# Kernel tuning notes

Measured on AMD Instinct MI355X. Metric: run time of the kernel, lower is better.

## Reference

```python
import jax, jax.numpy as jnp
import numpy as np

EPS = 1e-5

def layer_norm(x, g, b):
    mu = jnp.mean(x, axis=-1, keepdims=True)
    var = jnp.mean(jnp.square(x - mu), axis=-1, keepdims=True)
    return (x - mu) * jax.lax.rsqrt(var + EPS) * g + b

def gather_recent(seq_tokens, seq_mask, count):
    # vectorized right-aligned gather of last `count` valid tokens per row
    B, S, D = seq_tokens.shape
    csum = jnp.cumsum(seq_mask.astype(jnp.int32), axis=1)          # [B,S]
    total = csum[:, -1:]                                           # [B,1]
    rank = total - csum                                            # 0 = last valid (at valid positions)
    sel = seq_mask & (rank < count)
    dest = jnp.where(sel, count - 1 - rank, count)                 # dump invalid into slot `count`
    b_idx = jnp.arange(B)[:, None]
    buf = jnp.zeros((B, count + 1, D), seq_tokens.dtype)
    recent = buf.at[b_idx, dest].set(seq_tokens * sel[..., None].astype(seq_tokens.dtype))[:, :count]
    recent_mask = jnp.arange(count)[None, :] >= (count - total)    # [B,count]
    return recent, recent_mask

def setup_inputs() -> dict:
    key = jax.random.key(0)
    B, S, D, H, P = 16, 2048, 1024, 16, 8
    ks = jax.random.split(key, 8)
    hidden_states = jax.random.normal(ks[0], (B, S, D), jnp.float32)
    lengths = jax.random.randint(ks[1], (B,), 1, S + 1)
    valid_mask = jnp.arange(S)[None, :] < lengths[:, None]
    s = 0.02
    return {
        "hidden_states": hidden_states,
        "valid_mask": valid_mask,
        "queries": jax.random.normal(ks[2], (P, D), jnp.float32) * s,
        "in_proj_w": jax.random.normal(ks[3], (3 * D, D), jnp.float32) * s,
        "in_proj_b": jnp.zeros((3 * D,), jnp.float32),
        "out_w": jax.random.normal(ks[4], (D, D), jnp.float32) * s,
        "out_b": jnp.zeros((D,), jnp.float32),
        "ln_pma_g": jnp.ones((D,), jnp.float32),
        "ln_pma_b": jnp.zeros((D,), jnp.float32),
        "ln_v_g": jnp.ones((D,), jnp.float32),
        "ln_v_b": jnp.zeros((D,), jnp.float32),
        "W_v": jax.random.normal(ks[5], (D, D), jnp.float32) * s,
        "b_v": jnp.zeros((D,), jnp.float32),
        "ln_g_g": jnp.ones((D,), jnp.float32),
        "ln_g_b": jnp.zeros((D,), jnp.float32),
        "W_g": jax.random.normal(ks[6], (D, D), jnp.float32) * s,
        "b_g": jnp.zeros((D,), jnp.float32),
        "cls_count": 1, "pma_count": 8, "recent_count": 64, "num_heads": 16,
    }

def reference(hidden_states, valid_mask, queries, in_proj_w, in_proj_b, out_w, out_b,
              ln_pma_g, ln_pma_b, ln_v_g, ln_v_b, W_v, b_v, ln_g_g, ln_g_b, W_g, b_g,
              cls_count, pma_count, recent_count, num_heads):
    B, S, D = hidden_states.shape
    H = num_heads
    hd = D // H
    # ---- PMA (torch nn.MultiheadAttention, batch_first, eval/no-dropout) ----
    Wq, Wk, Wv_ = in_proj_w[:D], in_proj_w[D:2 * D], in_proj_w[2 * D:]
    bq, bk, bv_ = in_proj_b[:D], in_proj_b[D:2 * D], in_proj_b[2 * D:]
    q = (queries @ Wq.T + bq)                       # [P, D]
    k = hidden_states @ Wk.T + bk                   # [B, S, D]
    v = hidden_states @ Wv_.T + bv_                 # [B, S, D]
    qh = q.reshape(pma_count, H, hd)                # [P, H, hd]
    kh = k.reshape(B, S, H, hd)
    vh = v.reshape(B, S, H, hd)
    scores = jnp.einsum('phd,bshd->bhps', qh, kh) / jnp.sqrt(jnp.asarray(hd, hidden_states.dtype))
    scores = jnp.where(valid_mask[:, None, None, :], scores, jnp.asarray(-1e9, scores.dtype))
    attn = jax.nn.softmax(scores, axis=-1)          # [B, H, P, S]
    ctx = jnp.einsum('bhps,bshd->bphd', attn, vh).reshape(B, pma_count, D)
    pooled = ctx @ out_w.T + out_b
    pma_tokens = layer_norm(queries[None, :, :] + pooled, ln_pma_g, ln_pma_b)  # [B, P, D]
    pma_mask = jnp.ones((B, pma_count), bool)
    # ---- split cls / sequence, gather recent ----
    cls_tokens = hidden_states[:, :cls_count]
    cls_mask = valid_mask[:, :cls_count]
    recent_tokens, recent_mask = gather_recent(hidden_states[:, cls_count:],
                                               valid_mask[:, cls_count:], recent_count)
    summary = jnp.concatenate([cls_tokens, pma_tokens, recent_tokens], axis=1)
    summary_mask = jnp.concatenate([cls_mask, pma_mask, recent_mask], axis=1)
    # ---- SiLU self-gating ----
    val = jax.nn.silu(layer_norm(summary, ln_v_g, ln_v_b) @ W_v.T + b_v)
    gate = jax.nn.sigmoid(layer_norm(summary, ln_g_g, ln_g_b) @ W_g.T + b_g)
    gated = gate * val * summary_mask[..., None].astype(summary.dtype)
    return gated, summary_mask
```

## Files before the change

kernel.cpp:

```cpp
#include <hip/hip_runtime.h>
#include <hip/hip_bf16.h>
#include <math.h>


#define Bn 16
#define Sn 2048
#define Dn 1024
#define Hn 16
#define Pn 8
#define Tn 73
#define RECn 64

typedef __attribute__((ext_vector_type(8))) short short8;
typedef __attribute__((ext_vector_type(4))) float f32x4;

__device__ __forceinline__ short f2bf(float x) {
    union { __hip_bfloat16 h; short s; } u;
    u.h = __float2bfloat16(x);
    return u.s;
}

__global__ void detect_mask_kernel(const unsigned char* __restrict__ raw,
                                   int* __restrict__ flag) {
    __shared__ int any;
    if (threadIdx.x == 0) any = 0;
    __syncthreads();
    const uint4* r4 = (const uint4*)raw;
    int local = 0;
    for (int i = threadIdx.x; i < (Bn * Sn) / 16; i += blockDim.x) {
        uint4 w = r4[i];
        if ((w.x & 0xFFFFFF00u) | (w.y & 0xFFFFFF00u) |
            (w.z & 0xFFFFFF00u) | (w.w & 0xFFFFFF00u)) local = 1;
    }
    if (local) any = 1;
    __syncthreads();
    if (threadIdx.x == 0) *flag = any;
}

__global__ void canon_mask_kernel(const void* __restrict__ raw,
                                  const int* __restrict__ flag,
                                  unsigned char* __restrict__ canon) {
    int i = blockIdx.x * blockDim.x + threadIdx.x;
    if (i >= Bn * Sn) return;
    unsigned char v;
    if (*flag)
        v = ((const unsigned char*)raw)[i] ? 1 : 0;
    else
        v = ((const int*)raw)[i] ? 1 : 0;
    canon[i] = v;
}

__global__ void prep_kernel(const unsigned char* __restrict__ valid,
                            int* __restrict__ totals, int* __restrict__ rsrc,
                            float* __restrict__ maskf) {
    int b = blockIdx.x, t = threadIdx.x;
    const int SP = Sn - 1;
    __shared__ int lc[256];
    if (t < RECn) rsrc[b * RECn + t] = -1;

    int base = t * 8;
    unsigned char m[8];
    int cnt = 0;
#pragma unroll
    for (int i = 0; i < 8; i++) {
        int idx = base + i;
        m[i] = (idx < SP) ? valid[(size_t)b * Sn + 1 + idx] : (unsigned char)0;
        cnt += m[i] ? 1 : 0;
    }
    lc[t] = cnt;
    __syncthreads();
    for (int off = 1; off < 256; off <<= 1) {
        int add = (t >= off) ? lc[t - off] : 0;
        __syncthreads();
        lc[t] += add;
        __syncthreads();
    }
    int total = lc[255];
    int run = lc[t] - cnt;
#pragma unroll
    for (int i = 0; i < 8; i++) {
        if (m[i]) {
            run++;
            int rank = total - run;
            if (rank < RECn) rsrc[b * RECn + (RECn - 1 - rank)] = base + i + 1;
        }
    }
    if (t == 0) totals[b] = total;
    if (t < Tn) {
        float mv;
        if (t == 0) mv = valid[(size_t)b * Sn] ? 1.0f : 0.0f;
        else if (t < 1 + Pn) mv = 1.0f;
        else mv = ((t - 9) >= RECn - total) ? 1.0f : 0.0f;
        maskf[b * Tn + t] = mv;
    }
}

__global__ void q_kernel(const float* __restrict__ queries,
                         const float* __restrict__ in_w,
                         const float* __restrict__ in_b,
                         float* __restrict__ q) {
    int wid = (blockIdx.x * blockDim.x + threadIdx.x) >> 6;
    int lane = threadIdx.x & 63;
    if (wid >= Pn * Dn) return;
    int p = wid >> 10, j = wid & 1023;
    float acc = 0.0f;
    for (int c = lane; c < Dn; c += 64)
        acc += queries[p * Dn + c] * in_w[(size_t)j * Dn + c];
#pragma unroll
    for (int off = 32; off > 0; off >>= 1) acc += __shfl_down(acc, off);
    if (lane == 0) q[wid] = acc + in_b[j];
}

__global__ void A_kernel(const float* __restrict__ q,
                         const float* __restrict__ in_w,
                         const float* __restrict__ in_b,
                         short* __restrict__ Amat_bf, float* __restrict__ c0) {
    int h = blockIdx.x, cblk = blockIdx.y;
    int c = cblk * 256 + threadIdx.x;
    __shared__ float qs[8][64];
    for (int i = threadIdx.x; i < 512; i += 256) {
        int p = i >> 6, d = i & 63;
        qs[p][d] = q[p * Dn + h * 64 + d];
    }
    __syncthreads();
    float acc[8] = {};
#pragma unroll 8
    for (int d = 0; d < 64; d++) {
        float w = in_w[(size_t)(Dn + h * 64 + d) * Dn + c];
#pragma unroll
        for (int p = 0; p < 8; p++) acc[p] = fmaf(qs[p][d], w, acc[p]);
    }
#pragma unroll
    for (int p = 0; p < 8; p++)
        Amat_bf[(size_t)(h * 8 + p) * Dn + c] = f2bf(acc[p] * 0.125f);
    if (cblk == 0 && threadIdx.x < 8) {
        int p = threadIdx.x;
        float a = 0.0f;
        for (int d = 0; d < 64; d++) a += qs[p][d] * in_b[Dn + h * 64 + d];
        c0[h * 8 + p] = a * 0.125f;
    }
}

__global__ void wcvt_kernel(const float* __restrict__ w, short* __restrict__ wbf, int n) {
    int i = (blockIdx.x * blockDim.x + threadIdx.x) * 8;
    if (i >= n) return;
    f32x4 x0 = *(const f32x4*)(w + i);
    f32x4 x1 = *(const f32x4*)(w + i + 4);
    short8 o;
#pragma unroll
    for (int j = 0; j < 4; j++) { o[j] = f2bf(x0[j]); o[j + 4] = f2bf(x1[j]); }
    *(short8*)(wbf + i) = o;
}

__global__ __launch_bounds__(256) void scores_mfma(const float* __restrict__ hidden,
                                                   const short* __restrict__ Amat_bf,
                                                   const float* __restrict__ c0,
                                                   const unsigned char* __restrict__ valid,
                                                   float* __restrict__ scores) {
    int tid = threadIdx.x, wave = tid >> 6, lane = tid & 63;
    int l15 = lane & 15, koff = (lane >> 4) * 8;
    int mrow0 = blockIdx.x * 32 + (wave >> 1) * 16;
    int hpbase = (wave & 1) * 64;
    int b = mrow0 >> 11, s_base = mrow0 & 2047;

    __shared__ short Ab[2][128][40];
    int shp = tid >> 1, skp = (tid & 1) * 16;
    const short* aglob = Amat_bf + (size_t)shp * Dn + skp;
    const float* hptr = hidden + (size_t)(mrow0 + l15) * Dn + koff;

    f32x4 acc[4] = {};
    {
        short8 s0 = *(const short8*)(aglob);
        short8 s1 = *(const short8*)(aglob + 8);
        *(short8*)(&Ab[0][shp][skp]) = s0;
        *(short8*)(&Ab[0][shp][skp + 8]) = s1;
    }
    f32x4 ha = *(const f32x4*)(hptr);
    f32x4 hb = *(const f32x4*)(hptr + 4);
    f32x4 ha1 = *(const f32x4*)(hptr + 32);
    f32x4 hb1 = *(const f32x4*)(hptr + 36);

    for (int ic = 0; ic < 32; ic++) {
        int cur = ic & 1;
        short8 nA0 = {}, nA1 = {};
        f32x4 nh0 = {}, nh1 = {};
        if (ic + 1 < 32) {
            nA0 = *(const short8*)(aglob + (ic + 1) * 32);
            nA1 = *(const short8*)(aglob + (ic + 1) * 32 + 8);
        }
        if (ic + 2 < 32) {
            nh0 = *(const f32x4*)(hptr + (ic + 2) * 32);
            nh1 = *(const f32x4*)(hptr + (ic + 2) * 32 + 4);
        }
        __syncthreads();
        short8 av;
#pragma unroll
        for (int i = 0; i < 4; i++) { av[i] = f2bf(ha[i]); av[i + 4] = f2bf(hb[i]); }
#pragma unroll
        for (int nt = 0; nt < 4; nt++) {
            short8 bv = *(const short8*)(&Ab[cur][hpbase + nt * 16 + l15][koff]);
            acc[nt] = __builtin_amdgcn_mfma_f32_16x16x32_bf16(av, bv, acc[nt], 0, 0, 0);
        }
        if (ic + 1 < 32) {
            *(short8*)(&Ab[cur ^ 1][shp][skp]) = nA0;
            *(short8*)(&Ab[cur ^ 1][shp][skp + 8]) = nA1;
        }
        ha = ha1; hb = hb1; ha1 = nh0; hb1 = nh1;
    }
    int srow = s_base + (lane >> 4) * 4;
    const unsigned char* vptr = valid + (size_t)b * Sn + srow;
    bool ok0 = vptr[0] != 0, ok1 = vptr[1] != 0, ok2 = vptr[2] != 0, ok3 = vptr[3] != 0;
#pragma unroll
    for (int nt = 0; nt < 4; nt++) {
        int hp = hpbase + nt * 16 + l15;
        float cc = c0[hp];
        f32x4 st;
        st[0] = ok0 ? acc[nt][0] + cc : -1.0e9f;
        st[1] = ok1 ? acc[nt][1] + cc : -1.0e9f;
        st[2] = ok2 ? acc[nt][2] + cc : -1.0e9f;
        st[3] = ok3 ? acc[nt][3] + cc : -1.0e9f;
        *(f32x4*)(scores + (size_t)(b * 128 + hp) * Sn + srow) = st;
    }
}

__global__ __launch_bounds__(256) void softmax_kernel(const float* __restrict__ scores,
                                                      short* __restrict__ attn_bf) {
    const float* row = scores + (size_t)blockIdx.x * Sn;
    short* orow = attn_bf + (size_t)blockIdx.x * Sn;
    int t = threadIdx.x;
    __shared__ float red[256];
    f32x4 v0 = *(const f32x4*)(row + t * 8);
    f32x4 v1 = *(const f32x4*)(row + t * 8 + 4);
    float mx = -1.0e30f;
#pragma unroll
    for (int i = 0; i < 4; i++) { mx = fmaxf(mx, v0[i]); mx = fmaxf(mx, v1[i]); }
    red[t] = mx;
    __syncthreads();
    for (int off = 128; off > 0; off >>= 1) {
        if (t < off) red[t] = fmaxf(red[t], red[t + off]);
        __syncthreads();
    }
    mx = red[0];
    __syncthreads();
    float e[8];
    float sum = 0.0f;
#pragma unroll
    for (int i = 0; i < 4; i++) {
        e[i] = expf(v0[i] - mx); sum += e[i];
        e[i + 4] = expf(v1[i] - mx); sum += e[i + 4];
    }
    red[t] = sum;
    __syncthreads();
    for (int off = 128; off > 0; off >>= 1) {
        if (t < off) red[t] += red[t + off];
        __syncthreads();
    }
    float inv = 1.0f / red[0];
    short8 o;
#pragma unroll
    for (int i = 0; i < 8; i++) o[i] = f2bf(e[i] * inv);
    *(short8*)(orow + t * 8) = o;
}

__global__ __launch_bounds__(512) void U_mfma(const short* __restrict__ attn_bf,
                                              const float* __restrict__ hidden,
                                              float* __restrict__ Up0,
                                              float* __restrict__ Up1,
                                              float* __restrict__ Up2,
                                              float* __restrict__ Up3) {
    int b = blockIdx.y, n0 = blockIdx.x * 128, z = blockIdx.z;
    int zbase = z * 512;
    float* Up = (z == 0) ? Up0 : (z == 1) ? Up1 : (z == 2) ? Up2 : Up3;

    int tid = threadIdx.x, wave = tid >> 6, lane = tid & 63;
    int l15 = lane & 15;
    __shared__ short ldsB[2][128][40];
    int kr = tid & 31, nc = (tid >> 5) * 8;
    int koff = (lane >> 4) * 8;
    f32x4 acc[8] = {};
    const short* aBase = attn_bf + ((size_t)b * 128 + wave * 16 + l15) * Sn + zbase + koff;
    const float* hBase = hidden + ((size_t)b * Sn + zbase + kr) * Dn + n0 + nc;

    const int nk = 16;
    f32x4 h0 = *(const f32x4*)(hBase);
    f32x4 h1 = *(const f32x4*)(hBase + 4);
#pragma unroll
    for (int i = 0; i < 4; i++) {
        ldsB[0][nc + i][kr] = f2bf(h0[i]);
        ldsB[0][nc + 4 + i][kr] = f2bf(h1[i]);
    }
    short8 av = *(const short8*)(aBase);

    for (int ic = 0; ic < nk; ic++) {
        int cur = ic & 1;
        bool more = (ic + 1 < nk);
        f32x4 hn0, hn1;
        short8 avn;
        if (more) {
            hn0 = *(const f32x4*)(hBase + (size_t)(ic + 1) * 32 * Dn);
            hn1 = *(const f32x4*)(hBase + (size_t)(ic + 1) * 32 * Dn + 4);
            avn = *(const short8*)(aBase + (ic + 1) * 32);
        }
        __syncthreads();
#pragma unroll
        for (int nf = 0; nf < 8; nf++) {
            short8 bv = *(const short8*)(&ldsB[cur][nf * 16 + l15][koff]);
            acc[nf] = __builtin_amdgcn_mfma_f32_16x16x32_bf16(av, bv, acc[nf], 0, 0, 0);
        }
        if (more) {
#pragma unroll
            for (int i = 0; i < 4; i++) {
                ldsB[cur ^ 1][nc + i][kr] = f2bf(hn0[i]);
                ldsB[cur ^ 1][nc + 4 + i][kr] = f2bf(hn1[i]);
            }
            av = avn;
        }
    }
    int hp = wave * 16 + (lane >> 4) * 4;
#pragma unroll
    for (int nf = 0; nf < 8; nf++) {
        int c = n0 + nf * 16 + l15;
        float* up = Up + (size_t)(b * 128 + hp) * Dn + c;
#pragma unroll
        for (int r = 0; r < 4; r++) up[(size_t)r * Dn] = acc[nf][r];
    }
}

__global__ __launch_bounds__(64) void ctx_mfma(const float* __restrict__ Up0,
                                               const float* __restrict__ Up1,
                                               const float* __restrict__ Up2,
                                               const float* __restrict__ Up3,
                                               const float* __restrict__ in_w,
                                               const float* __restrict__ in_b,
                                               float* __restrict__ ctx) {
    int bh = blockIdx.x, b = bh >> 4, h = bh & 15;
    int lane = threadIdx.x & 63, l15 = lane & 15, koff = (lane >> 4) * 8;
    int p = l15 & 7;
    size_t uoff = ((size_t)b * 128 + h * 8 + p) * Dn + koff;
    const float* wv = in_w + (size_t)(2 * Dn + h * 64 + l15) * Dn + koff;
    f32x4 acc[4] = {};
    for (int k0 = 0; k0 < Dn; k0 += 32) {
        f32x4 a0 = *(const f32x4*)(Up0 + uoff + k0);
        f32x4 a1 = *(const f32x4*)(Up0 + uoff + k0 + 4);
        f32x4 b0 = *(const f32x4*)(Up1 + uoff + k0);
        f32x4 b1 = *(const f32x4*)(Up1 + uoff + k0 + 4);
        f32x4 d0 = *(const f32x4*)(Up2 + uoff + k0);
        f32x4 d1 = *(const f32x4*)(Up2 + uoff + k0 + 4);
        f32x4 e0 = *(const f32x4*)(Up3 + uoff + k0);
        f32x4 e1 = *(const f32x4*)(Up3 + uoff + k0 + 4);
        short8 av;
#pragma unroll
        for (int i = 0; i < 4; i++) {
            av[i] = f2bf((a0[i] + b0[i]) + (d0[i] + e0[i]));
            av[i + 4] = f2bf((a1[i] + b1[i]) + (d1[i] + e1[i]));
        }
#pragma unroll
        for (int nt = 0; nt < 4; nt++) {
            f32x4 w0 = *(const f32x4*)(wv + (size_t)nt * 16 * Dn + k0);
            f32x4 w1 = *(const f32x4*)(wv + (size_t)nt * 16 * Dn + k0 + 4);
            short8 bv;
#pragma unroll
            for (int i = 0; i < 4; i++) { bv[i] = f2bf(w0[i]); bv[i + 4] = f2bf(w1[i]); }
            acc[nt] = __builtin_amdgcn_mfma_f32_16x16x32_bf16(av, bv, acc[nt], 0, 0, 0);
        }
    }
    if (lane < 32) {
        int prow = (lane >> 4) * 4;
#pragma unroll
        for (int nt = 0; nt < 4; nt++) {
            int d = h * 64 + nt * 16 + l15;
            float bias = in_b[2 * Dn + d];
#pragma unroll
            for (int r = 0; r < 4; r++)
                ctx[(size_t)(b * 8 + prow + r) * Dn + d] = acc[nt][r] + bias;
        }
    }
}

__global__ __launch_bounds__(256) void pooled_mfma(const float* __restrict__ A,
                                                   const float* __restrict__ B,
                                                   const float* __restrict__ bias,
                                                   float* __restrict__ C, int M) {
    int wave = threadIdx.x >> 6, lane = threadIdx.x & 63;
    int l15 = lane & 15, koff = (lane >> 4) * 8;
    int m0 = blockIdx.x * 64 + (wave >> 1) * 32;
    int n0 = blockIdx.y * 64 + (wave & 1) * 32;
    f32x4 acc[2][2] = {};
    int ra0 = min(m0 + l15, M - 1);
    int ra1 = min(m0 + 16 + l15, M - 1);
    const float* a0p = A + (size_t)ra0 * Dn + koff;
    const float* a1p = A + (size_t)ra1 * Dn + koff;
    const float* b0p = B + (size_t)(n0 + l15) * Dn + koff;
    const float* b1p = B + (size_t)(n0 + 16 + l15) * Dn + koff;
    for (int k0 = 0; k0 < Dn; k0 += 32) {
        short8 av0, av1, bv0, bv1;
        f32x4 x, y;
        x = *(const f32x4*)(a0p + k0); y = *(const f32x4*)(a0p + k0 + 4);
#pragma unroll
        for (int i = 0; i < 4; i++) { av0[i] = f2bf(x[i]); av0[i + 4] = f2bf(y[i]); }
        x = *(const f32x4*)(a1p + k0); y = *(const f32x4*)(a1p + k0 + 4);
#pragma unroll
        for (int i = 0; i < 4; i++) { av1[i] = f2bf(x[i]); av1[i + 4] = f2bf(y[i]); }
        x = *(const f32x4*)(b0p + k0); y = *(const f32x4*)(b0p + k0 + 4);
#pragma unroll
        for (int i = 0; i < 4; i++) { bv0[i] = f2bf(x[i]); bv0[i + 4] = f2bf(y[i]); }
        x = *(const f32x4*)(b1p + k0); y = *(const f32x4*)(b1p + k0 + 4);
#pragma unroll
        for (int i = 0; i < 4; i++) { bv1[i] = f2bf(x[i]); bv1[i + 4] = f2bf(y[i]); }
        acc[0][0] = __builtin_amdgcn_mfma_f32_16x16x32_bf16(av0, bv0, acc[0][0], 0, 0, 0);
        acc[0][1] = __builtin_amdgcn_mfma_f32_16x16x32_bf16(av0, bv1, acc[0][1], 0, 0, 0);
        acc[1][0] = __builtin_amdgcn_mfma_f32_16x16x32_bf16(av1, bv0, acc[1][0], 0, 0, 0);
        acc[1][1] = __builtin_amdgcn_mfma_f32_16x16x32_bf16(av1, bv1, acc[1][1], 0, 0, 0);
    }
#pragma unroll
    for (int mf = 0; mf < 2; mf++) {
        int row0 = m0 + mf * 16 + (lane >> 4) * 4;
#pragma unroll
        for (int nf = 0; nf < 2; nf++) {
            int col = n0 + nf * 16 + l15;
            float bval = bias[col];
#pragma unroll
            for (int r = 0; r < 4; r++) {
                int row = row0 + r;
                if (row < M) C[(size_t)row * Dn + col] = acc[mf][nf][r] + bval;
            }
        }
    }
}

__global__ __launch_bounds__(256) void wgemm_mfma(const short* __restrict__ Abf,
                                                  const short* __restrict__ Bbf,
                                                  const float* __restrict__ bias,
                                                  float* __restrict__ C, int M) {
    int wave = threadIdx.x >> 6, lane = threadIdx.x & 63;
    int m0 = blockIdx.x * 64 + (wave >> 1) * 32;
    int n0 = blockIdx.y * 64 + (wave & 1) * 32;
    int koff = (lane >> 4) * 8;
    f32x4 acc[2][2] = {};
    int ra0 = min(m0 + (lane & 15), M - 1);
    int ra1 = min(m0 + 16 + (lane & 15), M - 1);
    const short* a0p = Abf + (size_t)ra0 * Dn + koff;
    const short* a1p = Abf + (size_t)ra1 * Dn + koff;
    const short* b0p = Bbf + (size_t)(n0 + (lane & 15)) * Dn + koff;
    const short* b1p = Bbf + (size_t)(n0 + 16 + (lane & 15)) * Dn + koff;
    for (int k0 = 0; k0 < Dn; k0 += 32) {
        short8 av0 = *(const short8*)(a0p + k0);
        short8 av1 = *(const short8*)(a1p + k0);
        short8 bv0 = *(const short8*)(b0p + k0);
        short8 bv1 = *(const short8*)(b1p + k0);
        acc[0][0] = __builtin_amdgcn_mfma_f32_16x16x32_bf16(av0, bv0, acc[0][0], 0, 0, 0);
        acc[0][1] = __builtin_amdgcn_mfma_f32_16x16x32_bf16(av0, bv1, acc[0][1], 0, 0, 0);
        acc[1][0] = __builtin_amdgcn_mfma_f32_16x16x32_bf16(av1, bv0, acc[1][0], 0, 0, 0);
        acc[1][1] = __builtin_amdgcn_mfma_f32_16x16x32_bf16(av1, bv1, acc[1][1], 0, 0, 0);
    }
#pragma unroll
    for (int mf = 0; mf < 2; mf++) {
        int row0 = m0 + mf * 16 + (lane >> 4) * 4;
#pragma unroll
        for (int nf = 0; nf < 2; nf++) {
            int col = n0 + nf * 16 + (lane & 15);
            float bval = bias[col];
#pragma unroll
            for (int r = 0; r < 4; r++) {
                int row = row0 + r;
                if (row < M) C[(size_t)row * Dn + col] = acc[mf][nf][r] + bval;
            }
        }
    }
}

__device__ __forceinline__ float block_sum(float v, float* red) {
    int tid = threadIdx.x;
    red[tid] = v;
    __syncthreads();
    for (int off = 128; off > 0; off >>= 1) {
        if (tid < off) red[tid] += red[tid + off];
        __syncthreads();
    }
    float r = red[0];
    __syncthreads();
    return r;
}

__global__ void summary_ln_kernel(const float* __restrict__ hidden,
                                  const float* __restrict__ queries,
                                  const float* __restrict__ pooled,
                                  const int* __restrict__ rsrc,
                                  const float* __restrict__ gpma, const float* __restrict__ bpma,
                                  const float* __restrict__ gv, const float* __restrict__ bv,
                                  const float* __restrict__ gg, const float* __restrict__ bg,
                                  short* __restrict__ lnv, short* __restrict__ lng) {
    __shared__ float red[256];
    int b = blockIdx.x, t = blockIdx.y, tid = threadIdx.x;
    float x[4];
    if (t == 0) {
#pragma unroll
        for (int i = 0; i < 4; i++)
            x[i] = hidden[(size_t)b * Sn * Dn + tid + i * 256];
    } else if (t < 1 + Pn) {
        int p = t - 1;
#pragma unroll
        for (int i = 0; i < 4; i++) {
            int c = tid + i * 256;
            x[i] = queries[p * Dn + c] + pooled[((size_t)b * Pn + p) * Dn + c];
        }
    } else {
        int src = rsrc[b * RECn + (t - 9)];
        if (src >= 0) {
#pragma unroll
            for (int i = 0; i < 4; i++)
                x[i] = hidden[((size_t)b * Sn + src) * Dn + tid + i * 256];
        } else {
#pragma unroll
            for (int i = 0; i < 4; i++) x[i] = 0.0f;
        }
    }
    if (t >= 1 && t < 1 + Pn) {
        float mu = block_sum(x[0] + x[1] + x[2] + x[3], red) * (1.0f / Dn);
        float d2 = 0.0f;
#pragma unroll
        for (int i = 0; i < 4; i++) { float d = x[i] - mu; d2 += d * d; }
        float inv = rsqrtf(block_sum(d2, red) * (1.0f / Dn) + 1e-5f);
#pragma unroll
        for (int i = 0; i < 4; i++) {
            int c = tid + i * 256;
            x[i] = (x[i] - mu) * inv * gpma[c] + bpma[c];
        }
    }
    float mu = block_sum(x[0] + x[1] + x[2] + x[3], red) * (1.0f / Dn);
    float d2 = 0.0f;
#pragma unroll
    for (int i = 0; i < 4; i++) { float d = x[i] - mu; d2 += d * d; }
    float inv = rsqrtf(block_sum(d2, red) * (1.0f / Dn) + 1e-5f);
    size_t row = (size_t)(b * Tn + t) * Dn;
#pragma unroll
    for (int i = 0; i < 4; i++) {
        int c = tid + i * 256;
        float xh = (x[i] - mu) * inv;
        lnv[row + c] = f2bf(xh * gv[c] + bv[c]);
        lng[row + c] = f2bf(xh * gg[c] + bg[c]);
    }
}

__global__ void gated_kernel(const float* __restrict__ c1, const float* __restrict__ c2,
                             const float* __restrict__ maskf, float* __restrict__ out) {
    int gi = blockIdx.x * blockDim.x + threadIdx.x;
    int row = gi >> 10;
    float m = maskf[row];
    float a = c1[gi], g = c2[gi];
    float sv = a / (1.0f + expf(-a));
    float sg = 1.0f / (1.0f + expf(-g));
    out[gi] = sg * sv * m;
}

extern "C" void kernel_launch(void* const* d_in, const int* in_sizes, int n_in,
                              void* d_out, int out_size, void* d_ws, size_t ws_size,
                              hipStream_t stream) {
    const float* hidden = (const float*)d_in[0];
    const void* valid_raw = d_in[1];
    const float* queries = (const float*)d_in[2];
    const float* in_w = (const float*)d_in[3];
    const float* in_b = (const float*)d_in[4];
    const float* out_w = (const float*)d_in[5];
    const float* out_b = (const float*)d_in[6];
    const float* ln_pma_g = (const float*)d_in[7];
    const float* ln_pma_b = (const float*)d_in[8];
    const float* ln_v_g = (const float*)d_in[9];
    const float* ln_v_b = (const float*)d_in[10];
    const float* W_v = (const float*)d_in[11];
    const float* b_v = (const float*)d_in[12];
    const float* ln_g_g = (const float*)d_in[13];
    const float* ln_g_b = (const float*)d_in[14];
    const float* W_g = (const float*)d_in[15];
    const float* b_g = (const float*)d_in[16];

    float* ws = (float*)d_ws;
    float* out = (float*)d_out;

    float* SC      = ws;
    short* attn_bf = (short*)(ws + 4194304);
    float* Up0     = ws + 6291456;
    float* Up1     = ws;
    float* Up2     = ws + 2097152;
    float* Up3     = ws + 8388608;
    float* qbuf    = ws + 10485760;
    short* Amat_bf = (short*)(ws + 10493952);
    float* c0      = ws + 10559488;
    float* ctx     = ws + 10559744;
    float* pooled  = ws + 10690816;
    short* Wv_bf   = (short*)(ws + 10821888);
    short* Wg_bf   = (short*)(ws + 11346176);
    int*   ivals   = (int*)(ws + 11870464);
    int* totals = ivals;
    int* rsrc = ivals + 16;
    int* flag = ivals + 16 + 1024;
    unsigned char* canon = (unsigned char*)(ivals + 16 + 1024 + 16);
    short* lnv_bf = (short*)ws;
    short* lng_bf = (short*)(ws + 622592);
    float* c1 = ws + 1245184;
    float* c2 = ws + 2441216;
    float* maskf = out + (size_t)Bn * Tn * Dn;

    const int M2 = Bn * Tn;

    detect_mask_kernel<<<1, 256, 0, stream>>>((const unsigned char*)valid_raw, flag);
    canon_mask_kernel<<<(Bn * Sn) / 256, 256, 0, stream>>>(valid_raw, flag, canon);
    prep_kernel<<<Bn, 256, 0, stream>>>(canon, totals, rsrc, maskf);
    q_kernel<<<(Pn * Dn) / 4, 256, 0, stream>>>(queries, in_w, in_b, qbuf);
    A_kernel<<<dim3(Hn, 4), 256, 0, stream>>>(qbuf, in_w, in_b, Amat_bf, c0);
    wcvt_kernel<<<512, 256, 0, stream>>>(W_v, Wv_bf, Dn * Dn);
    wcvt_kernel<<<512, 256, 0, stream>>>(W_g, Wg_bf, Dn * Dn);
    scores_mfma<<<(Bn * Sn) / 32, 256, 0, stream>>>(hidden, Amat_bf, c0, canon, SC);
    softmax_kernel<<<Bn * 128, 256, 0, stream>>>(SC, attn_bf);
    U_mfma<<<dim3(8, Bn, 4), 512, 0, stream>>>(attn_bf, hidden, Up0, Up1, Up2, Up3);
    ctx_mfma<<<Bn * Hn, 64, 0, stream>>>(Up0, Up1, Up2, Up3, in_w, in_b, ctx);
    pooled_mfma<<<dim3(2, 16), 256, 0, stream>>>(ctx, out_w, out_b, pooled, Bn * Pn);
    summary_ln_kernel<<<dim3(Bn, Tn), 256, 0, stream>>>(hidden, queries, pooled, rsrc,
                                                        ln_pma_g, ln_pma_b, ln_v_g, ln_v_b,
                                                        ln_g_g, ln_g_b, lnv_bf, lng_bf);
    wgemm_mfma<<<dim3((M2 + 63) / 64, 16), 256, 0, stream>>>(lnv_bf, Wv_bf, b_v, c1, M2);
    wgemm_mfma<<<dim3((M2 + 63) / 64, 16), 256, 0, stream>>>(lng_bf, Wg_bf, b_g, c2, M2);
    gated_kernel<<<(Bn * Tn * Dn) / 256, 256, 0, stream>>>(c1, c2, maskf, out);
}
```

Before: 260.2 us.

## Stage full K-half tiles in swizzled LDS for scores and U GEMMs

scores_mfma now runs as a split-K GEMM over two halves with 512 threads. It loads the whole 128x512 bf16 A-matrix slice into XOR-swizzled shared memory once, writes two partial score buffers, and leaves the bias add and masking to the softmax kernel. U_mfma similarly converts and stages its entire 512x128 hidden tile into swizzled LDS up front, replacing the per-step double-buffered loop with its barriers. This drops per-iteration syncs and bank conflicts and lets each block reuse more data. In exchange it uses 128 KB of LDS per block, which limits occupancy, and it adds extra partial-score traffic to global memory.

Result: faster. 249.2 us (-4.2%).

```diff
diff --git a/kernel.cpp b/kernel.cpp
--- a/kernel.cpp
+++ b/kernel.cpp
@@ -18,6 +18,10 @@
     union { __hip_bfloat16 h; short s; } u;
     u.h = __float2bfloat16(x);
     return u.s;
+}
+
+__device__ __forceinline__ int swz(int row, int ks) {
+    return row * 512 + (ks ^ ((row & 7) << 3));
 }
 
 __global__ void detect_mask_kernel(const unsigned char* __restrict__ raw,
@@ -152,88 +156,85 @@
     *(short8*)(wbf + i) = o;
 }
 
-__global__ __launch_bounds__(256) void scores_mfma(const float* __restrict__ hidden,
+__global__ __launch_bounds__(512) void scores_mfma(const float* __restrict__ hidden,
                                                    const short* __restrict__ Amat_bf,
-                                                   const float* __restrict__ c0,
-                                                   const unsigned char* __restrict__ valid,
-                                                   float* __restrict__ scores) {
+                                                   float* __restrict__ SCp0,
+                                                   float* __restrict__ SCp1) {
+    __shared__ short Bsh[128 * 512];
     int tid = threadIdx.x, wave = tid >> 6, lane = tid & 63;
-    int l15 = lane & 15, koff = (lane >> 4) * 8;
-    int mrow0 = blockIdx.x * 32 + (wave >> 1) * 16;
-    int hpbase = (wave & 1) * 64;
-    int b = mrow0 >> 11, s_base = mrow0 & 2047;
-
-    __shared__ short Ab[2][128][40];
-    int shp = tid >> 1, skp = (tid & 1) * 16;
-    const short* aglob = Amat_bf + (size_t)shp * Dn + skp;
-    const float* hptr = hidden + (size_t)(mrow0 + l15) * Dn + koff;
-
-    f32x4 acc[4] = {};
+    int l15 = lane & 15, q = lane >> 4;
+    int kz = blockIdx.y, khalf = kz << 9;
+    float* SCp = kz ? SCp1 : SCp0;
+    int m0 = blockIdx.x * 128 + wave * 16;
+    int b = m0 >> 11, s_base = m0 & 2047;
+
     {
-        short8 s0 = *(const short8*)(aglob);
-        short8 s1 = *(const short8*)(aglob + 8);
-        *(short8*)(&Ab[0][shp][skp]) = s0;
-        *(short8*)(&Ab[0][shp][skp + 8]) = s1;
-    }
-    f32x4 ha = *(const f32x4*)(hptr);
-    f32x4 hb = *(const f32x4*)(hptr + 4);
-    f32x4 ha1 = *(const f32x4*)(hptr + 32);
-    f32x4 hb1 = *(const f32x4*)(hptr + 36);
-
-    for (int ic = 0; ic < 32; ic++) {
-        int cur = ic & 1;
-        short8 nA0 = {}, nA1 = {};
-        f32x4 nh0 = {}, nh1 = {};
-        if (ic + 1 < 32) {
-            nA0 = *(const short8*)(aglob + (ic + 1) * 32);
-            nA1 = *(const short8*)(aglob + (ic + 1) * 32 + 8);
-        }
-        if (ic + 2 < 32) {
-            nh0 = *(const f32x4*)(hptr + (ic + 2) * 32);
-            nh1 = *(const f32x4*)(hptr + (ic + 2) * 32 + 4);
-        }
-        __syncthreads();
+        int r = tid >> 2, k0 = (tid & 3) * 128;
+        const short* src = Amat_bf + (size_t)r * Dn + khalf + k0;
+#pragma unroll
+        for (int j = 0; j < 16; j++) {
+            short8 v = *(const short8*)(src + j * 8);
+            *(short8*)(&Bsh[swz(r, k0 + j * 8)]) = v;
+        }
+    }
+    __syncthreads();
+
+    const float* aptr = hidden + (size_t)(m0 + l15) * Dn + khalf + q * 8;
+    f32x4 acc[8] = {};
+    f32x4 pa[2][2];
+    pa[0][0] = *(const f32x4*)(aptr);       pa[0][1] = *(const f32x4*)(aptr + 4);
+    pa[1][0] = *(const f32x4*)(aptr + 32);  pa[1][1] = *(const f32x4*)(aptr + 36);
+#pragma unroll 4
+    for (int ic = 0; ic < 16; ic++) {
+        f32x4 c0r = pa[ic & 1][0], c1r = pa[ic & 1][1];
+        if (ic + 2 < 16) {
+            pa[ic & 1][0] = *(const f32x4*)(aptr + (ic + 2) * 32);
+            pa[ic & 1][1] = *(const f32x4*)(aptr + (ic + 2) * 32 + 4);
+        }
         short8 av;
 #pragma unroll
-        for (int i = 0; i < 4; i++) { av[i] = f2bf(ha[i]); av[i + 4] = f2bf(hb[i]); }
-#pragma unroll
-        for (int nt = 0; nt < 4; nt++) {
-            short8 bv = *(const short8*)(&Ab[cur][hpbase + nt * 16 + l15][koff]);
+        for (int i = 0; i < 4; i++) { av[i] = f2bf(c0r[i]); av[i + 4] = f2bf(c1r[i]); }
+#pragma unroll
+        for (int nt = 0; nt < 8; nt++) {
+            short8 bv = *(const short8*)(&Bsh[swz(nt * 16 + l15, ic * 32 + q * 8)]);
             acc[nt] = __builtin_amdgcn_mfma_f32_16x16x32_bf16(av, bv, acc[nt], 0, 0, 0);
         }
-        if (ic + 1 < 32) {
-            *(short8*)(&Ab[cur ^ 1][shp][skp]) = nA0;
-            *(short8*)(&Ab[cur ^ 1][shp][skp + 8]) = nA1;
-        }
-        ha = ha1; hb = hb1; ha1 = nh0; hb1 = nh1;
-    }
-    int srow = s_base + (lane >> 4) * 4;
-    const unsigned char* vptr = valid + (size_t)b * Sn + srow;
-    bool ok0 = vptr[0] != 0, ok1 = vptr[1] != 0, ok2 = vptr[2] != 0, ok3 = vptr[3] != 0;
-#pragma unroll
-    for (int nt = 0; nt < 4; nt++) {
-        int hp = hpbase + nt * 16 + l15;
-        float cc = c0[hp];
-        f32x4 st;
-        st[0] = ok0 ? acc[nt][0] + cc : -1.0e9f;
-        st[1] = ok1 ? acc[nt][1] + cc : -1.0e9f;
-        st[2] = ok2 ? acc[nt][2] + cc : -1.0e9f;
-        st[3] = ok3 ? acc[nt][3] + cc : -1.0e9f;
-        *(f32x4*)(scores + (size_t)(b * 128 + hp) * Sn + srow) = st;
-    }
-}
-
-__global__ __launch_bounds__(256) void softmax_kernel(const float* __restrict__ scores,
+    }
+    int srow = s_base + q * 4;
+#pragma unroll
+    for (int nt = 0; nt < 8; nt++) {
+        int hp = nt * 16 + l15;
+        *(f32x4*)(SCp + (size_t)(b * 128 + hp) * Sn + srow) = acc[nt];
+    }
+}
+
+__global__ __launch_bounds__(256) void softmax_kernel(const float* __restrict__ p0,
+                                                      const float* __restrict__ p1,
+                                                      const float* __restrict__ c0,
+                                                      const unsigned char* __restrict__ valid,
                                                       short* __restrict__ attn_bf) {
-    const float* row = scores + (size_t)blockIdx.x * Sn;
-    short* orow = attn_bf + (size_t)blockIdx.x * Sn;
+    int rowid = blockIdx.x;
+    int b = rowid >> 7, hp = rowid & 127;
+    const float* r0 = p0 + (size_t)rowid * Sn;
+    const float* r1 = p1 + (size_t)rowid * Sn;
+    const unsigned char* vp = valid + (size_t)b * Sn;
+    short* orow = attn_bf + (size_t)rowid * Sn;
     int t = threadIdx.x;
+    float cc = c0[hp];
     __shared__ float red[256];
-    f32x4 v0 = *(const f32x4*)(row + t * 8);
-    f32x4 v1 = *(const f32x4*)(row + t * 8 + 4);
+    f32x4 a0 = *(const f32x4*)(r0 + t * 8);
+    f32x4 a1 = *(const f32x4*)(r0 + t * 8 + 4);
+    f32x4 b0 = *(const f32x4*)(r1 + t * 8);
+    f32x4 b1 = *(const f32x4*)(r1 + t * 8 + 4);
+    float v[8];
+#pragma unroll
+    for (int i = 0; i < 4; i++) {
+        v[i] = (vp[t * 8 + i] != 0) ? (a0[i] + b0[i] + cc) : -1.0e9f;
+        v[i + 4] = (vp[t * 8 + 4 + i] != 0) ? (a1[i] + b1[i] + cc) : -1.0e9f;
+    }
     float mx = -1.0e30f;
 #pragma unroll
-    for (int i = 0; i < 4; i++) { mx = fmaxf(mx, v0[i]); mx = fmaxf(mx, v1[i]); }
+    for (int i = 0; i < 8; i++) mx = fmaxf(mx, v[i]);
     red[t] = mx;
     __syncthreads();
     for (int off = 128; off > 0; off >>= 1) {
@@ -242,13 +243,9 @@
     }
     mx = red[0];
     __syncthreads();
-    float e[8];
     float sum = 0.0f;
 #pragma unroll
-    for (int i = 0; i < 4; i++) {
-        e[i] = expf(v0[i] - mx); sum += e[i];
-        e[i + 4] = expf(v1[i] - mx); sum += e[i + 4];
-    }
+    for (int i = 0; i < 8; i++) { v[i] = expf(v[i] - mx); sum += v[i]; }
     red[t] = sum;
     __syncthreads();
     for (int off = 128; off > 0; off >>= 1) {
@@ -258,7 +255,7 @@
     float inv = 1.0f / red[0];
     short8 o;
 #pragma unroll
-    for (int i = 0; i < 8; i++) o[i] = f2bf(e[i] * inv);
+    for (int i = 0; i < 8; i++) o[i] = f2bf(v[i] * inv);
     *(short8*)(orow + t * 8) = o;
 }
 
@@ -268,55 +265,47 @@
                                               float* __restrict__ Up1,
                                               float* __restrict__ Up2,
                                               float* __restrict__ Up3) {
-    int b = blockIdx.y, n0 = blockIdx.x * 128, z = blockIdx.z;
+    __shared__ short Hs[128 * 512];
+    int n0 = blockIdx.x * 128, b = blockIdx.y, z = blockIdx.z;
     int zbase = z * 512;
     float* Up = (z == 0) ? Up0 : (z == 1) ? Up1 : (z == 2) ? Up2 : Up3;
-
     int tid = threadIdx.x, wave = tid >> 6, lane = tid & 63;
-    int l15 = lane & 15;
-    __shared__ short ldsB[2][128][40];
-    int kr = tid & 31, nc = (tid >> 5) * 8;
-    int koff = (lane >> 4) * 8;
+    int l15 = lane & 15, q = lane >> 4;
+
+    {
+        const float* src = hidden + ((size_t)b * Sn + zbase + tid) * Dn + n0;
+#pragma unroll 4
+        for (int c = 0; c < 128; c += 8) {
+            f32x4 x = *(const f32x4*)(src + c);
+            f32x4 y = *(const f32x4*)(src + c + 4);
+#pragma unroll
+            for (int i = 0; i < 4; i++) {
+                Hs[swz(c + i, 0) + ((tid ^ (((c + i) & 7) << 3)) - (0 ^ (((c + i) & 7) << 3)))] = f2bf(x[i]);
+            }
+#pragma unroll
+            for (int i = 0; i < 4; i++) {
+                Hs[(c + 4 + i) * 512 + (tid ^ (((c + 4 + i) & 7) << 3))] = f2bf(y[i]);
+            }
+        }
+    }
+    __syncthreads();
+
+    const short* ap = attn_bf + ((size_t)b * 128 + wave * 16 + l15) * Sn + zbase + q * 8;
     f32x4 acc[8] = {};
-    const short* aBase = attn_bf + ((size_t)b * 128 + wave * 16 + l15) * Sn + zbase + koff;
-    const float* hBase = hidden + ((size_t)b * Sn + zbase + kr) * Dn + n0 + nc;
-
-    const int nk = 16;
-    f32x4 h0 = *(const f32x4*)(hBase);
-    f32x4 h1 = *(const f32x4*)(hBase + 4);
-#pragma unroll
-    for (int i = 0; i < 4; i++) {
-        ldsB[0][nc + i][kr] = f2bf(h0[i]);
-        ldsB[0][nc + 4 + i][kr] = f2bf(h1[i]);
-    }
-    short8 av = *(const short8*)(aBase);
-
-    for (int ic = 0; ic < nk; ic++) {
-        int cur = ic & 1;
-        bool more = (ic + 1 < nk);
-        f32x4 hn0, hn1;
-        short8 avn;
-        if (more) {
-            hn0 = *(const f32x4*)(hBase + (size_t)(ic + 1) * 32 * Dn);
-            hn1 = *(const f32x4*)(hBase + (size_t)(ic + 1) * 32 * Dn + 4);
-            avn = *(const short8*)(aBase + (ic + 1) * 32);
-        }
-        __syncthreads();
+    short8 pa[2];
+    pa[0] = *(const short8*)(ap);
+    pa[1] = *(const short8*)(ap + 32);
+#pragma unroll 4
+    for (int ic = 0; ic < 16; ic++) {
+        short8 av = pa[ic & 1];
+        if (ic + 2 < 16) pa[ic & 1] = *(const short8*)(ap + (ic + 2) * 32);
 #pragma unroll
         for (int nf = 0; nf < 8; nf++) {
-            short8 bv = *(const short8*)(&ldsB[cur][nf * 16 + l15][koff]);
+            short8 bv = *(const short8*)(&Hs[swz(nf * 16 + l15, ic * 32 + q * 8)]);
             acc[nf] = __builtin_amdgcn_mfma_f32_16x16x32_bf16(av, bv, acc[nf], 0, 0, 0);
         }
-        if (more) {
-#pragma unroll
-            for (int i = 0; i < 4; i++) {
-                ldsB[cur ^ 1][nc + i][kr] = f2bf(hn0[i]);
-                ldsB[cur ^ 1][nc + 4 + i][kr] = f2bf(hn1[i]);
-            }
-            av = avn;
-        }
-    }
-    int hp = wave * 16 + (lane >> 4) * 4;
+    }
+    int hp = wave * 16 + q * 4;
 #pragma unroll
     for (int nf = 0; nf < 8; nf++) {
         int c = n0 + nf * 16 + l15;
@@ -577,12 +566,13 @@
     float* ws = (float*)d_ws;
     float* out = (float*)d_out;
 
-    float* SC      = ws;
-    short* attn_bf = (short*)(ws + 4194304);
-    float* Up0     = ws + 6291456;
-    float* Up1     = ws;
-    float* Up2     = ws + 2097152;
-    float* Up3     = ws + 8388608;
+    float* SCp0    = ws;
+    float* SCp1    = ws + 4194304;
+    short* attn_bf = (short*)(ws + 8388608);
+    float* Up0     = ws;
+    float* Up1     = ws + 2097152;
+    float* Up2     = ws + 4194304;
+    float* Up3     = ws + 6291456;
     float* qbuf    = ws + 10485760;
     short* Amat_bf = (short*)(ws + 10493952);
     float* c0      = ws + 10559488;
@@ -610,8 +600,8 @@
     A_kernel<<<dim3(Hn, 4), 256, 0, stream>>>(qbuf, in_w, in_b, Amat_bf, c0);
     wcvt_kernel<<<512, 256, 0, stream>>>(W_v, Wv_bf, Dn * Dn);
     wcvt_kernel<<<512, 256, 0, stream>>>(W_g, Wg_bf, Dn * Dn);
-    scores_mfma<<<(Bn * Sn) / 32, 256, 0, stream>>>(hidden, Amat_bf, c0, canon, SC);
-    softmax_kernel<<<Bn * 128, 256, 0, stream>>>(SC, attn_bf);
+    scores_mfma<<<dim3(256, 2), 512, 0, stream>>>(hidden, Amat_bf, SCp0, SCp1);
+    softmax_kernel<<<Bn * 128, 256, 0, stream>>>(SCp0, SCp1, c0, canon, attn_bf);
     U_mfma<<<dim3(8, Bn, 4), 512, 0, stream>>>(attn_bf, hidden, Up0, Up1, Up2, Up3);
     ctx_mfma<<<Bn * Hn, 64, 0, stream>>>(Up0, Up1, Up2, Up3, in_w, in_b, ctx);
     pooled_mfma<<<dim3(2, 16), 256, 0, stream>>>(ctx, out_w, out_b, pooled, Bn * Pn);
```

## Retile scores and U GEMMs with large swizzled LDS tiles and deeper prefetch

Applied to the files above, without the earlier changes.

The scores GEMM now uses 512-thread blocks covering 128 rows. Each block stages a 256-wide K slab of the bf16 query-key matrix in XOR-swizzled LDS, double-buffered, and prefetches the hidden-state A operand four K-steps ahead. The U GEMM now converts a whole 512x64 hidden tile to bf16 in swizzled LDS once, then streams the attention rows from registers, with no per-step barriers. The aim is fewer syncs, fewer LDS bank conflicts and more reuse per block, at the cost of much larger LDS use per block (128KB and 64KB), which limits occupancy. The Up buffer aliasing in the workspace is also rearranged.

Result: faster. 254.1 us (-2.3%).

```diff
diff --git a/kernel.cpp b/kernel.cpp
--- a/kernel.cpp
+++ b/kernel.cpp
@@ -18,6 +18,10 @@
     union { __hip_bfloat16 h; short s; } u;
     u.h = __float2bfloat16(x);
     return u.s;
+}
+
+__device__ __forceinline__ int swzP(int row, int ks, int pitch) {
+    return row * pitch + (ks ^ ((row & 7) << 3));
 }
 
 __global__ void detect_mask_kernel(const unsigned char* __restrict__ raw,
@@ -152,67 +156,78 @@
     *(short8*)(wbf + i) = o;
 }
 
-__global__ __launch_bounds__(256) void scores_mfma(const float* __restrict__ hidden,
+__global__ __launch_bounds__(512) void scores_mfma(const float* __restrict__ hidden,
                                                    const short* __restrict__ Amat_bf,
                                                    const float* __restrict__ c0,
                                                    const unsigned char* __restrict__ valid,
                                                    float* __restrict__ scores) {
+    __shared__ short Bsh[2][64 * 512];
     int tid = threadIdx.x, wave = tid >> 6, lane = tid & 63;
-    int l15 = lane & 15, koff = (lane >> 4) * 8;
-    int mrow0 = blockIdx.x * 32 + (wave >> 1) * 16;
-    int hpbase = (wave & 1) * 64;
-    int b = mrow0 >> 11, s_base = mrow0 & 2047;
-
-    __shared__ short Ab[2][128][40];
-    int shp = tid >> 1, skp = (tid & 1) * 16;
-    const short* aglob = Amat_bf + (size_t)shp * Dn + skp;
-    const float* hptr = hidden + (size_t)(mrow0 + l15) * Dn + koff;
-
-    f32x4 acc[4] = {};
+    int l15 = lane & 15, q = lane >> 4;
+    int m0 = blockIdx.x * 128 + wave * 16;
+    int b = m0 >> 11, s_base = m0 & 2047;
+
+    int sr = tid >> 2, skc = (tid & 3) * 64;
+    const short* aglob = Amat_bf + (size_t)sr * Dn + skc;
+
     {
-        short8 s0 = *(const short8*)(aglob);
-        short8 s1 = *(const short8*)(aglob + 8);
-        *(short8*)(&Ab[0][shp][skp]) = s0;
-        *(short8*)(&Ab[0][shp][skp + 8]) = s1;
-    }
-    f32x4 ha = *(const f32x4*)(hptr);
-    f32x4 hb = *(const f32x4*)(hptr + 4);
-    f32x4 ha1 = *(const f32x4*)(hptr + 32);
-    f32x4 hb1 = *(const f32x4*)(hptr + 36);
-
-    for (int ic = 0; ic < 32; ic++) {
-        int cur = ic & 1;
-        short8 nA0 = {}, nA1 = {};
-        f32x4 nh0 = {}, nh1 = {};
-        if (ic + 1 < 32) {
-            nA0 = *(const short8*)(aglob + (ic + 1) * 32);
-            nA1 = *(const short8*)(aglob + (ic + 1) * 32 + 8);
-        }
-        if (ic + 2 < 32) {
-            nh0 = *(const f32x4*)(hptr + (ic + 2) * 32);
-            nh1 = *(const f32x4*)(hptr + (ic + 2) * 32 + 4);
-        }
-        __syncthreads();
-        short8 av;
-#pragma unroll
-        for (int i = 0; i < 4; i++) { av[i] = f2bf(ha[i]); av[i + 4] = f2bf(hb[i]); }
-#pragma unroll
-        for (int nt = 0; nt < 4; nt++) {
-            short8 bv = *(const short8*)(&Ab[cur][hpbase + nt * 16 + l15][koff]);
-            acc[nt] = __builtin_amdgcn_mfma_f32_16x16x32_bf16(av, bv, acc[nt], 0, 0, 0);
-        }
-        if (ic + 1 < 32) {
-            *(short8*)(&Ab[cur ^ 1][shp][skp]) = nA0;
-            *(short8*)(&Ab[cur ^ 1][shp][skp + 8]) = nA1;
-        }
-        ha = ha1; hb = hb1; ha1 = nh0; hb1 = nh1;
-    }
-    int srow = s_base + (lane >> 4) * 4;
+#pragma unroll
+        for (int j = 0; j < 8; j++) {
+            short8 v = *(const short8*)(aglob + j * 8);
+            *(short8*)(&Bsh[0][swzP(sr, skc + j * 8, 256)]) = v;
+        }
+    }
+    __syncthreads();
+
+    const float* aptr = hidden + (size_t)(m0 + l15) * Dn + q * 8;
+    f32x4 acc[8] = {};
+    f32x4 pa[4][2];
+#pragma unroll
+    for (int d = 0; d < 4; d++) {
+        pa[d][0] = *(const f32x4*)(aptr + d * 32);
+        pa[d][1] = *(const f32x4*)(aptr + d * 32 + 4);
+    }
+
+    for (int kq = 0; kq < 4; kq++) {
+        int cur = kq & 1;
+        short8 sreg[8];
+        if (kq < 3) {
+            const short* src = aglob + (kq + 1) * 256;
+#pragma unroll
+            for (int j = 0; j < 8; j++) sreg[j] = *(const short8*)(src + j * 8);
+        }
+#pragma unroll
+        for (int icq = 0; icq < 8; icq++) {
+            int ic = kq * 8 + icq;
+            f32x4 h0 = pa[icq & 3][0], h1 = pa[icq & 3][1];
+            if (ic + 4 < 32) {
+                pa[icq & 3][0] = *(const f32x4*)(aptr + (ic + 4) * 32);
+                pa[icq & 3][1] = *(const f32x4*)(aptr + (ic + 4) * 32 + 4);
+            }
+            short8 av;
+#pragma unroll
+            for (int i = 0; i < 4; i++) { av[i] = f2bf(h0[i]); av[i + 4] = f2bf(h1[i]); }
+#pragma unroll
+            for (int nt = 0; nt < 8; nt++) {
+                short8 bv = *(const short8*)(&Bsh[cur][swzP(nt * 16 + l15, icq * 32 + q * 8, 256)]);
+                acc[nt] = __builtin_amdgcn_mfma_f32_16x16x32_bf16(av, bv, acc[nt], 0, 0, 0);
+            }
+        }
+        if (kq < 3) {
+            __syncthreads();
+#pragma unroll
+            for (int j = 0; j < 8; j++)
+                *(short8*)(&Bsh[cur ^ 1][swzP(sr, skc + j * 8, 256)]) = sreg[j];
+            __syncthreads();
+        }
+    }
+
+    int srow = s_base + q * 4;
     const unsigned char* vptr = valid + (size_t)b * Sn + srow;
     bool ok0 = vptr[0] != 0, ok1 = vptr[1] != 0, ok2 = vptr[2] != 0, ok3 = vptr[3] != 0;
 #pragma unroll
-    for (int nt = 0; nt < 4; nt++) {
-        int hp = hpbase + nt * 16 + l15;
+    for (int nt = 0; nt < 8; nt++) {
+        int hp = nt * 16 + l15;
         float cc = c0[hp];
         f32x4 st;
         st[0] = ok0 ? acc[nt][0] + cc : -1.0e9f;
@@ -268,57 +283,51 @@
                                               float* __restrict__ Up1,
                                               float* __restrict__ Up2,
                                               float* __restrict__ Up3) {
-    int b = blockIdx.y, n0 = blockIdx.x * 128, z = blockIdx.z;
+    __shared__ short Hs[64 * 512];
+    int n0 = blockIdx.x * 64, b = blockIdx.y, z = blockIdx.z;
     int zbase = z * 512;
     float* Up = (z == 0) ? Up0 : (z == 1) ? Up1 : (z == 2) ? Up2 : Up3;
-
     int tid = threadIdx.x, wave = tid >> 6, lane = tid & 63;
-    int l15 = lane & 15;
-    __shared__ short ldsB[2][128][40];
-    int kr = tid & 31, nc = (tid >> 5) * 8;
-    int koff = (lane >> 4) * 8;
-    f32x4 acc[8] = {};
-    const short* aBase = attn_bf + ((size_t)b * 128 + wave * 16 + l15) * Sn + zbase + koff;
-    const float* hBase = hidden + ((size_t)b * Sn + zbase + kr) * Dn + n0 + nc;
-
-    const int nk = 16;
-    f32x4 h0 = *(const f32x4*)(hBase);
-    f32x4 h1 = *(const f32x4*)(hBase + 4);
-#pragma unroll
-    for (int i = 0; i < 4; i++) {
-        ldsB[0][nc + i][kr] = f2bf(h0[i]);
-        ldsB[0][nc + 4 + i][kr] = f2bf(h1[i]);
-    }
-    short8 av = *(const short8*)(aBase);
-
-    for (int ic = 0; ic < nk; ic++) {
-        int cur = ic & 1;
-        bool more = (ic + 1 < nk);
-        f32x4 hn0, hn1;
-        short8 avn;
-        if (more) {
-            hn0 = *(const f32x4*)(hBase + (size_t)(ic + 1) * 32 * Dn);
-            hn1 = *(const f32x4*)(hBase + (size_t)(ic + 1) * 32 * Dn + 4);
-            avn = *(const short8*)(aBase + (ic + 1) * 32);
-        }
-        __syncthreads();
-#pragma unroll
-        for (int nf = 0; nf < 8; nf++) {
-            short8 bv = *(const short8*)(&ldsB[cur][nf * 16 + l15][koff]);
+    int l15 = lane & 15, q = lane >> 4;
+
+    {
+        const float* src = hidden + ((size_t)b * Sn + zbase + tid) * Dn + n0;
+#pragma unroll
+        for (int c8 = 0; c8 < 64; c8 += 8) {
+            f32x4 x = *(const f32x4*)(src + c8);
+            f32x4 y = *(const f32x4*)(src + c8 + 4);
+#pragma unroll
+            for (int i = 0; i < 4; i++) {
+                int c = c8 + i;
+                Hs[c * 512 + (tid ^ ((c & 7) << 3))] = f2bf(x[i]);
+            }
+#pragma unroll
+            for (int i = 0; i < 4; i++) {
+                int c = c8 + 4 + i;
+                Hs[c * 512 + (tid ^ ((c & 7) << 3))] = f2bf(y[i]);
+            }
+        }
+    }
+    __syncthreads();
+
+    const short* ap = attn_bf + ((size_t)b * 128 + wave * 16 + l15) * Sn + zbase + q * 8;
+    f32x4 acc[4] = {};
+    short8 pa4[4];
+#pragma unroll
+    for (int d = 0; d < 4; d++) pa4[d] = *(const short8*)(ap + d * 32);
+#pragma unroll
+    for (int ic = 0; ic < 16; ic++) {
+        short8 av = pa4[ic & 3];
+        if (ic + 4 < 16) pa4[ic & 3] = *(const short8*)(ap + (ic + 4) * 32);
+#pragma unroll
+        for (int nf = 0; nf < 4; nf++) {
+            short8 bv = *(const short8*)(&Hs[swzP(nf * 16 + l15, ic * 32 + q * 8, 512)]);
             acc[nf] = __builtin_amdgcn_mfma_f32_16x16x32_bf16(av, bv, acc[nf], 0, 0, 0);
         }
-        if (more) {
-#pragma unroll
-            for (int i = 0; i < 4; i++) {
-                ldsB[cur ^ 1][nc + i][kr] = f2bf(hn0[i]);
-                ldsB[cur ^ 1][nc + 4 + i][kr] = f2bf(hn1[i]);
-            }
-            av = avn;
-        }
-    }
-    int hp = wave * 16 + (lane >> 4) * 4;
-#pragma unroll
-    for (int nf = 0; nf < 8; nf++) {
+    }
+    int hp = wave * 16 + q * 4;
+#pragma unroll
+    for (int nf = 0; nf < 4; nf++) {
         int c = n0 + nf * 16 + l15;
         float* up = Up + (size_t)(b * 128 + hp) * Dn + c;
 #pragma unroll
@@ -579,9 +588,9 @@
 
     float* SC      = ws;
     short* attn_bf = (short*)(ws + 4194304);
-    float* Up0     = ws + 6291456;
-    float* Up1     = ws;
-    float* Up2     = ws + 2097152;
+    float* Up0     = ws;
+    float* Up1     = ws + 2097152;
+    float* Up2     = ws + 6291456;
     float* Up3     = ws + 8388608;
     float* qbuf    = ws + 10485760;
     short* Amat_bf = (short*)(ws + 10493952);
@@ -610,9 +619,9 @@
     A_kernel<<<dim3(Hn, 4), 256, 0, stream>>>(qbuf, in_w, in_b, Amat_bf, c0);
     wcvt_kernel<<<512, 256, 0, stream>>>(W_v, Wv_bf, Dn * Dn);
     wcvt_kernel<<<512, 256, 0, stream>>>(W_g, Wg_bf, Dn * Dn);
-    scores_mfma<<<(Bn * Sn) / 32, 256, 0, stream>>>(hidden, Amat_bf, c0, canon, SC);
+    scores_mfma<<<(Bn * Sn) / 128, 512, 0, stream>>>(hidden, Amat_bf, c0, canon, SC);
     softmax_kernel<<<Bn * 128, 256, 0, stream>>>(SC, attn_bf);
-    U_mfma<<<dim3(8, Bn, 4), 512, 0, stream>>>(attn_bf, hidden, Up0, Up1, Up2, Up3);
+    U_mfma<<<dim3(16, Bn, 4), 512, 0, stream>>>(attn_bf, hidden, Up0, Up1, Up2, Up3);
     ctx_mfma<<<Bn * Hn, 64, 0, stream>>>(Up0, Up1, Up2, Up3, in_w, in_b, ctx);
     pooled_mfma<<<dim3(2, 16), 256, 0, stream>>>(ctx, out_w, out_b, pooled, Bn * Pn);
     summary_ln_kernel<<<dim3(Bn, Tn), 256, 0, stream>>>(hidden, queries, pooled, rsrc,
```
